# Optimization experiments

Measured on AMD Instinct MI355X. Metric: run time of the kernel, lower is better.

## Reference

```python
import jax, jax.numpy as jnp
import numpy as np

B, I, H, O, T = 512, 512, 1024, 512, 128

def setup_inputs() -> dict:
    key = jax.random.key(0)
    ks = jax.random.split(key, 8)
    s_in = 1.0 / np.sqrt(I)
    s_h = 1.0 / np.sqrt(H)
    return {
        "x": jax.random.normal(ks[0], (B, I), dtype=jnp.float32),
        "h0": jnp.zeros((B, H), dtype=jnp.float32),
        "Wjx": jax.random.normal(ks[1], (H, I), dtype=jnp.float32) * s_in,
        "bjx": jnp.zeros((H,), dtype=jnp.float32),
        "Wjh": jax.random.normal(ks[2], (H, H), dtype=jnp.float32) * s_h,
        "bjh": jnp.zeros((H,), dtype=jnp.float32),
        "Wkx": jax.random.normal(ks[3], (H, I), dtype=jnp.float32) * s_in,
        "bkx": jnp.zeros((H,), dtype=jnp.float32),
        "Wkh": jax.random.normal(ks[4], (H, H), dtype=jnp.float32) * s_h,
        "bkh": jnp.zeros((H,), dtype=jnp.float32),
        "Wo": jax.random.normal(ks[5], (O, H), dtype=jnp.float32) * s_h,
        "bo": jnp.zeros((O,), dtype=jnp.float32),
        "seq_length": T,
    }

def reference(x, h0, Wjx, bjx, Wjh, bjh, Wkx, bkx, Wkh, bkh, Wo, bo, seq_length):
    # x is broadcast to every timestep (original repeats x along time).
    # Precompute the time-invariant input projections once; same math.
    jx = x @ Wjx.T + bjx  # [B,H]
    kx = x @ Wkx.T + bkx  # [B,H]

    def step(h, _):
        j = jax.nn.sigmoid(jx + h @ Wjh.T + bjh)
        k = jax.nn.sigmoid(kx + h @ Wkh.T + bkh)
        new_h = j * (1.0 - h) + (1.0 - k) * h
        out = new_h @ Wo.T + bo  # [B,O]
        return new_h, out

    h_final, outs = jax.lax.scan(step, h0, None, length=seq_length)
    outputs = jnp.transpose(outs, (1, 0, 2))  # [B,T,O]
    return outputs, h_final
```

## Files before the change

kernel.cpp:

```cpp
#include <hip/hip_runtime.h>
#include <hip/hip_bf16.h>
#include <hip/hip_cooperative_groups.h>

namespace cg = cooperative_groups;

constexpr int B = 512;
constexpr int I = 512;
constexpr int H = 1024;
constexpr int O = 512;

using short8 = __attribute__((ext_vector_type(8))) short;
using f32x4  = __attribute__((ext_vector_type(4))) float;
using bf16_t = __hip_bfloat16;

__device__ __forceinline__ short8 ldfrag(const bf16_t* p) {
    return *reinterpret_cast<const short8*>(p);
}
__device__ __forceinline__ float sigmoid_f(float z) {
    return 1.0f / (1.0f + __expf(-z));
}

__device__ __forceinline__ void group_wait(int* c, int target) {
    if (threadIdx.x == 0) {
        while (__hip_atomic_load(c, __ATOMIC_RELAXED, __HIP_MEMORY_SCOPE_AGENT) < target)
            __builtin_amdgcn_s_sleep(2);
    }
    __syncthreads();
    asm volatile("buffer_inv sc0" ::: "memory");
}
__device__ __forceinline__ void group_post(int* c) {
    __syncthreads();
    if (threadIdx.x == 0)
        __hip_atomic_fetch_add(c, 1, __ATOMIC_RELAXED, __HIP_MEMORY_SCOPE_AGENT);
}

__global__ __launch_bounds__(256, 2)
void flipflop_rnn_kernel(const float* __restrict__ x,  const float* __restrict__ h0,
                         const float* __restrict__ Wjx, const float* __restrict__ bjx,
                         const float* __restrict__ Wjh, const float* __restrict__ bjh,
                         const float* __restrict__ Wkx, const float* __restrict__ bkx,
                         const float* __restrict__ Wkh, const float* __restrict__ bkh,
                         const float* __restrict__ Wo,  const float* __restrict__ bo,
                         const int* __restrict__ seqlen,
                         float* __restrict__ out,
                         bf16_t* __restrict__ wjh_bf, bf16_t* __restrict__ wkh_bf,
                         bf16_t* __restrict__ wo_bf,  bf16_t* __restrict__ wjx_bf,
                         bf16_t* __restrict__ wkx_bf, bf16_t* __restrict__ x_bf,
                         bf16_t* __restrict__ hbf0,   bf16_t* __restrict__ hbf1,
                         int* __restrict__ cnt)
{
    __shared__ short lds_w[32768];

    const int T    = seqlen[0];
    const int tid  = threadIdx.x;
    const int g    = blockIdx.x;
    const int nthr = gridDim.x * blockDim.x;
    const int gtid = g * blockDim.x + tid;

    for (int idx = gtid; idx < H * H; idx += nthr) wjh_bf[idx] = __float2bfloat16(Wjh[idx]);
    for (int idx = gtid; idx < H * H; idx += nthr) wkh_bf[idx] = __float2bfloat16(Wkh[idx]);
    for (int idx = gtid; idx < O * H; idx += nthr) wo_bf[idx]  = __float2bfloat16(Wo[idx]);
    for (int idx = gtid; idx < H * I; idx += nthr) wjx_bf[idx] = __float2bfloat16(Wjx[idx]);
    for (int idx = gtid; idx < H * I; idx += nthr) wkx_bf[idx] = __float2bfloat16(Wkx[idx]);
    for (int idx = gtid; idx < B * I; idx += nthr) x_bf[idx]   = __float2bfloat16(x[idx]);
    if (gtid < 8 * 256) cnt[gtid] = 0;

    const int w     = tid >> 6;
    const int lane  = tid & 63;
    const int quad  = lane >> 4;
    const int lm    = lane & 15;
    const int iblk  = g & 7;
    const int lblk  = g >> 3;
    const int rbase = iblk * 64 + w * 16;
    const int n0    = lblk * 16;
    const bool has_out = (lblk < 32);
    const int no0   = lblk * 16;
    int* grp_cnt = cnt + iblk * 256;

    float hreg[4];
    #pragma unroll
    for (int r = 0; r < 4; ++r) {
        const int row = rbase + quad * 4 + r;
        const int col = n0 + lm;
        const float hv = h0[row * H + col];
        hreg[r] = hv;
        hbf0[row * H + col] = __float2bfloat16(hv);
    }

    cg::this_grid().sync();

    for (int c = tid; c < 4096; c += 256) {
        const int gate = c >> 11;
        const int cc   = c & 2047;
        const int kb   = cc >> 4;
        const int col  = cc & 15;
        const bf16_t* src = (gate ? wkh_bf : wjh_bf) + (n0 + col) * H + kb * 8;
        *reinterpret_cast<short8*>(&lds_w[c * 8]) = *reinterpret_cast<const short8*>(src);
    }
    __syncthreads();

    float jxr[4], kxr[4];
    {
        f32x4 aJ = {0.f, 0.f, 0.f, 0.f};
        f32x4 aK = {0.f, 0.f, 0.f, 0.f};
        const bf16_t* aP = x_bf   + (rbase + lm) * I + quad * 8;
        const bf16_t* jP = wjx_bf + (n0 + lm) * I + quad * 8;
        const bf16_t* kP = wkx_bf + (n0 + lm) * I + quad * 8;
        #pragma unroll 4
        for (int k0 = 0; k0 < I; k0 += 32) {
            short8 a = ldfrag(aP + k0);
            aJ = __builtin_amdgcn_mfma_f32_16x16x32_bf16(a, ldfrag(jP + k0), aJ, 0, 0, 0);
            aK = __builtin_amdgcn_mfma_f32_16x16x32_bf16(a, ldfrag(kP + k0), aK, 0, 0, 0);
        }
        const int col = n0 + lm;
        #pragma unroll
        for (int r = 0; r < 4; ++r) {
            jxr[r] = aJ[r] + bjx[col] + bjh[col];
            kxr[r] = aK[r] + bkx[col] + bkh[col];
        }
    }
    const float bo_v = has_out ? bo[no0 + lm] : 0.0f;

    for (int t = 0; t < T; ++t) {
        if (t > 0) group_wait(grp_cnt + t, 64);
        const bf16_t* hb  = (t & 1) ? hbf1 : hbf0;
        bf16_t*       hbn = (t & 1) ? hbf0 : hbf1;

        f32x4 accJ = {0.f, 0.f, 0.f, 0.f};
        f32x4 accK = {0.f, 0.f, 0.f, 0.f};
        f32x4 accO = {0.f, 0.f, 0.f, 0.f};

        const bf16_t* aP = hb    + (rbase + lm) * H + quad * 8;
        const bf16_t* oP = wo_bf + (no0 + lm) * H + quad * 8;
        const short*  jL = lds_w + quad * 128 + lm * 8;
        const short*  kL = jL + 16384;

        if (has_out) {
            #pragma unroll 4
            for (int k0 = 0; k0 < H; k0 += 32) {
                short8 a  = ldfrag(aP + k0);
                short8 bj = *reinterpret_cast<const short8*>(jL + (k0 >> 3) * 128);
                short8 bk = *reinterpret_cast<const short8*>(kL + (k0 >> 3) * 128);
                accJ = __builtin_amdgcn_mfma_f32_16x16x32_bf16(a, bj, accJ, 0, 0, 0);
                accK = __builtin_amdgcn_mfma_f32_16x16x32_bf16(a, bk, accK, 0, 0, 0);
                accO = __builtin_amdgcn_mfma_f32_16x16x32_bf16(a, ldfrag(oP + k0), accO, 0, 0, 0);
            }
        } else {
            #pragma unroll 4
            for (int k0 = 0; k0 < H; k0 += 32) {
                short8 a  = ldfrag(aP + k0);
                short8 bj = *reinterpret_cast<const short8*>(jL + (k0 >> 3) * 128);
                short8 bk = *reinterpret_cast<const short8*>(kL + (k0 >> 3) * 128);
                accJ = __builtin_amdgcn_mfma_f32_16x16x32_bf16(a, bj, accJ, 0, 0, 0);
                accK = __builtin_amdgcn_mfma_f32_16x16x32_bf16(a, bk, accK, 0, 0, 0);
            }
        }

        if (has_out && t > 0) {
            #pragma unroll
            for (int r = 0; r < 4; ++r) {
                const int row = rbase + quad * 4 + r;
                out[(row * T + (t - 1)) * O + no0 + lm] = accO[r] + bo_v;
            }
        }

        #pragma unroll
        for (int r = 0; r < 4; ++r) {
            const int row = rbase + quad * 4 + r;
            const int col = n0 + lm;
            const float jv = sigmoid_f(accJ[r] + jxr[r]);
            const float kv = sigmoid_f(accK[r] + kxr[r]);
            const float hv = hreg[r];
            const float hn = jv * (1.0f - hv) + (1.0f - kv) * hv;
            hreg[r] = hn;
            hbn[row * H + col] = __float2bfloat16(hn);
        }

        group_post(grp_cnt + t + 1);
    }

    group_wait(grp_cnt + T, 64);

    {
        const bf16_t* hb = (T & 1) ? hbf1 : hbf0;
        if (has_out) {
            f32x4 accO = {0.f, 0.f, 0.f, 0.f};
            const bf16_t* aP = hb    + (rbase + lm) * H + quad * 8;
            const bf16_t* oP = wo_bf + (no0 + lm) * H + quad * 8;
            #pragma unroll 4
            for (int k0 = 0; k0 < H; k0 += 32) {
                accO = __builtin_amdgcn_mfma_f32_16x16x32_bf16(ldfrag(aP + k0), ldfrag(oP + k0), accO, 0, 0, 0);
            }
            #pragma unroll
            for (int r = 0; r < 4; ++r) {
                const int row = rbase + quad * 4 + r;
                out[(row * T + (T - 1)) * O + no0 + lm] = accO[r] + bo_v;
            }
        }
        const int hfin = B * T * O;
        #pragma unroll
        for (int r = 0; r < 4; ++r) {
            const int row = rbase + quad * 4 + r;
            const int col = n0 + lm;
            out[hfin + row * H + col] = hreg[r];
        }
    }
}

extern "C" void kernel_launch(void* const* d_in, const int* in_sizes, int n_in,
                              void* d_out, int out_size, void* d_ws, size_t ws_size,
                              hipStream_t stream) {
    const float* x   = (const float*)d_in[0];
    const float* h0  = (const float*)d_in[1];
    const float* Wjx = (const float*)d_in[2];
    const float* bjx = (const float*)d_in[3];
    const float* Wjh = (const float*)d_in[4];
    const float* bjh = (const float*)d_in[5];
    const float* Wkx = (const float*)d_in[6];
    const float* bkx = (const float*)d_in[7];
    const float* Wkh = (const float*)d_in[8];
    const float* bkh = (const float*)d_in[9];
    const float* Wo  = (const float*)d_in[10];
    const float* bo  = (const float*)d_in[11];
    const int* seqlen = (const int*)d_in[12];
    float* out = (float*)d_out;

    char* ws = (char*)d_ws;
    bf16_t* wjh_bf = (bf16_t*)(ws + 0);
    bf16_t* wkh_bf = (bf16_t*)(ws + 2097152);
    bf16_t* wo_bf  = (bf16_t*)(ws + 4194304);
    bf16_t* wjx_bf = (bf16_t*)(ws + 5242880);
    bf16_t* wkx_bf = (bf16_t*)(ws + 6291456);
    bf16_t* x_bf   = (bf16_t*)(ws + 7340032);
    bf16_t* hbf0   = (bf16_t*)(ws + 7864320);
    bf16_t* hbf1   = (bf16_t*)(ws + 8912896);
    int*    cnt    = (int*)   (ws + 9961472);

    void* args[] = {
        &x, &h0, &Wjx, &bjx, &Wjh, &bjh, &Wkx, &bkx, &Wkh, &bkh, &Wo, &bo,
        &seqlen, &out,
        &wjh_bf, &wkh_bf, &wo_bf, &wjx_bf, &wkx_bf, &x_bf, &hbf0, &hbf1, &cnt
    };
    hipLaunchCooperativeKernel((const void*)flipflop_rnn_kernel,
                               dim3(512), dim3(256), args, 0, stream);
}
```

Baseline: 1.995 ms.

## Replace per-step atomic counter barrier with per-block flag array polling

Swaps the per-timestep atomic counter, which one thread polls, for a flag array with one slot per block. Each block writes its step number to its own slot with sc0 and sc0-sc1 stores, and 64 threads poll all 64 slots in parallel, with a periodic fallback read that bypasses more of the cache. This removes the serialization of 64 atomic adds on one address and shortens the critical path of the per-step group barrier. It relies on the cache coherence behaviour of the sc bits, so stale reads could stall or break correctness if those semantics differ from what is assumed.

Result: slower. 2.741 ms (+37.4%).

```diff
diff --git a/kernel.cpp b/kernel.cpp
--- a/kernel.cpp
+++ b/kernel.cpp
@@ -20,18 +20,48 @@
     return 1.0f / (1.0f + __expf(-z));
 }
 
-__device__ __forceinline__ void group_wait(int* c, int target) {
-    if (threadIdx.x == 0) {
-        while (__hip_atomic_load(c, __ATOMIC_RELAXED, __HIP_MEMORY_SCOPE_AGENT) < target)
-            __builtin_amdgcn_s_sleep(2);
+__device__ __forceinline__ int load_sc0(const int* p) {
+    int v;
+    asm volatile("global_load_dword %0, %1, off sc0\n\t"
+                 "s_waitcnt vmcnt(0)"
+                 : "=v"(v) : "v"(p) : "memory");
+    return v;
+}
+__device__ __forceinline__ int load_sc01(const int* p) {
+    int v;
+    asm volatile("global_load_dword %0, %1, off sc0 sc1\n\t"
+                 "s_waitcnt vmcnt(0)"
+                 : "=v"(v) : "v"(p) : "memory");
+    return v;
+}
+
+__device__ __forceinline__ void group_wait(const int* grp, int target) {
+    if (threadIdx.x < 64) {
+        const int* lp = grp + threadIdx.x * 2;
+        const int* dp = grp + 128 + threadIdx.x * 2;
+        int it = 0;
+        while (load_sc0(lp) < target) {
+            ++it;
+            if ((it & 63) == 0) {
+                if (load_sc01(dp) >= target) break;
+            }
+            __builtin_amdgcn_s_sleep(1);
+        }
     }
     __syncthreads();
     asm volatile("buffer_inv sc0" ::: "memory");
 }
-__device__ __forceinline__ void group_post(int* c) {
+
+__device__ __forceinline__ void group_post(int* grp, int lblk, int value) {
     __syncthreads();
-    if (threadIdx.x == 0)
-        __hip_atomic_fetch_add(c, 1, __ATOMIC_RELAXED, __HIP_MEMORY_SCOPE_AGENT);
+    if (threadIdx.x == 0) {
+        int* lp = grp + lblk * 2;
+        int* dp = grp + 128 + lblk * 2;
+        asm volatile("global_store_dword %0, %1, off sc0"
+                     :: "v"(lp), "v"(value) : "memory");
+        asm volatile("global_store_dword %0, %1, off sc0 sc1"
+                     :: "v"(dp), "v"(value) : "memory");
+    }
 }
 
 __global__ __launch_bounds__(256, 2)
@@ -75,7 +105,7 @@
     const int n0    = lblk * 16;
     const bool has_out = (lblk < 32);
     const int no0   = lblk * 16;
-    int* grp_cnt = cnt + iblk * 256;
+    int* grp_flags = cnt + iblk * 256;
 
     float hreg[4];
     #pragma unroll
@@ -122,7 +152,7 @@
     const float bo_v = has_out ? bo[no0 + lm] : 0.0f;
 
     for (int t = 0; t < T; ++t) {
-        if (t > 0) group_wait(grp_cnt + t, 64);
+        if (t > 0) group_wait(grp_flags, t);
         const bf16_t* hb  = (t & 1) ? hbf1 : hbf0;
         bf16_t*       hbn = (t & 1) ? hbf0 : hbf1;
 
@@ -176,10 +206,10 @@
             hbn[row * H + col] = __float2bfloat16(hn);
         }
 
-        group_post(grp_cnt + t + 1);
-    }
-
-    group_wait(grp_cnt + T, 64);
+        group_post(grp_flags, lblk, t + 1);
+    }
+
+    group_wait(grp_flags, T);
 
     {
         const bf16_t* hb = (T & 1) ? hbf1 : hbf0;
```
